# Performance work log

Hardware: AMD Instinct MI355X
Metric: run time of the kernel (lower is better)

## Reference

```python
import jax, jax.numpy as jnp
import numpy as np

A0 = 0.5291772105638411
KE = 14.399645351950548
KEHALF = KE / 2.0

def softplus_inverse(x):
    x = np.asarray(x, dtype=np.float64)
    return np.float32(x + np.log(-np.expm1(-x)))

def setup_inputs() -> dict:
    key = jax.random.key(0)
    k1, k2, k3, k4 = jax.random.split(key, 4)
    B, N, K = 16, 8192, 128
    neighbors = jax.random.randint(k1, (B, N, K), 0, N, dtype=jnp.int64)
    neighbor_mask = jnp.ones((B, N, K), dtype=jnp.float32)
    # atomic numbers in [1, 94] (Z=0 would break d/dp of Z**p)
    atomic_numbers = jax.random.randint(k2, (B, N), 0, 94, dtype=jnp.int64) + 1
    # distances scaled into a physical range [0.5, 5.5) Angstrom to avoid r->0
    distances = jax.random.uniform(k3, (B, N, K), dtype=jnp.float32) * 5.0 + 0.5
    p = lambda v: jnp.full((1,), softplus_inverse(v), dtype=jnp.float32)
    return {
        'neighbors': neighbors,
        'neighbor_mask': neighbor_mask,
        'atomic_numbers': atomic_numbers,
        'distances': distances,
        'adiv': p(1.0 / (0.8854 * A0)),
        'apow': p(0.23),
        'c1': p(0.1818), 'c2': p(0.5099), 'c3': p(0.2802), 'c4': p(0.02817),
        'a1': p(3.2), 'a2': p(0.9423), 'a3': p(0.4028), 'a4': p(0.2016),
    }

def reference(neighbors, neighbor_mask, atomic_numbers, distances,
              adiv, apow, c1, c2, c3, c4, a1, a2, a3, a4):
    sp = jax.nn.softplus
    Zf = atomic_numbers.astype(jnp.float32)            # [B, N]
    zpow = Zf ** sp(apow)                              # [B, N]
    # per-batch gather over neighbor index (sparse edge list, no NxN build)
    gather = jax.vmap(lambda v, nb: v[nb])             # ([N],[N,K]) -> [N,K]
    zpow_j = gather(zpow, neighbors)                   # [B, N, K]
    a = (zpow[:, :, None] + zpow_j) * sp(adiv) * neighbor_mask
    zizj = Zf[:, :, None] * gather(Zf, neighbors) * neighbor_mask
    c1s, c2s, c3s, c4s = sp(c1), sp(c2), sp(c3), sp(c4)
    csum = c1s + c2s + c3s + c4s
    f = (c1s / csum) * jnp.exp(-sp(a1) * a * distances) \
      + (c2s / csum) * jnp.exp(-sp(a2) * a * distances) \
      + (c3s / csum) * jnp.exp(-sp(a3) * a * distances) \
      + (c4s / csum) * jnp.exp(-sp(a4) * a * distances)
    corr = jnp.where(neighbor_mask != 0,
                     KEHALF * f * zizj / distances,
                     jnp.zeros_like(distances))        # [B, N, K]
    return jnp.sum(corr, axis=(-1, -2))[:, None]       # [B, 1]
```

## Files before the change

### kernel.cpp

```cpp
#include <hip/hip_runtime.h>


#define KEHALF_F 7.199822675975274f
#define LOG2E_F  1.4426950408889634f
#define EPI      256
#define WAVES_PB 2
#define BUFB     3072

__device__ __forceinline__ float softplus_f(float x) {
    return (x > 20.f) ? x : log1pf(__expf(x));
}

__global__ void zbl_pre(const int* __restrict__ zn,
                        const float* __restrict__ adiv,
                        const float* __restrict__ apow,
                        const float* __restrict__ c1, const float* __restrict__ c2,
                        const float* __restrict__ c3, const float* __restrict__ c4,
                        const float* __restrict__ a1, const float* __restrict__ a2,
                        const float* __restrict__ a3, const float* __restrict__ a4,
                        unsigned short* __restrict__ packed, float* __restrict__ scal,
                        int total_atoms)
{
    int i = blockIdx.x * blockDim.x + threadIdx.x;
    const float spa = softplus_f(apow[0]);
    const float sad = softplus_f(adiv[0]);
    const float qb  = sad;
    const float qmax = sad * __expf(spa * __logf(94.f));
    const float qs  = (qmax - qb) * (1.f / 511.f);
    if (i == 0) {
        float s1 = softplus_f(c1[0]), s2 = softplus_f(c2[0]);
        float s3 = softplus_f(c3[0]), s4 = softplus_f(c4[0]);
        float inv = KEHALF_F / (s1 + s2 + s3 + s4);
        scal[0] = sad;
        scal[1] = s1 * inv;
        scal[2] = s2 * inv;
        scal[3] = s3 * inv;
        scal[4] = s4 * inv;
        scal[5] = -softplus_f(a1[0]) * LOG2E_F;
        scal[6] = -softplus_f(a2[0]) * LOG2E_F;
        scal[7] = -softplus_f(a3[0]) * LOG2E_F;
        scal[8] = -softplus_f(a4[0]) * LOG2E_F;
        scal[9]  = qb;
        scal[10] = qs;
    }
    if (i < total_atoms) {
        unsigned int Z = (unsigned int)zn[i];
        float Zf = (float)Z;
        float zps = sad * __expf(spa * __logf(Zf));
        float qf = (zps - qb) / qs;
        int q = (int)(qf + 0.5f);
        if (q < 0) q = 0;
        if (q > 511) q = 511;
        packed[i] = (unsigned short)(((unsigned)q << 7) | (Z & 0x7Fu));
    }
}

extern __shared__ unsigned short tab[];

#define STAGE(bufp, it) do {                                                      \
    const int*   _n = nb + (size_t)(it) * EPI + lane * 4;                         \
    const float* _m = mk + (size_t)(it) * EPI + lane * 4;                         \
    const float* _d = ds + (size_t)(it) * EPI + lane * 4;                         \
    __builtin_amdgcn_global_load_lds(                                             \
        (const __attribute__((address_space(1))) void*)_n,                        \
        (__attribute__((address_space(3))) void*)(bufp), 16, 0, 0);               \
    __builtin_amdgcn_global_load_lds(                                             \
        (const __attribute__((address_space(1))) void*)_m,                        \
        (__attribute__((address_space(3))) void*)((bufp) + 1024), 16, 0, 0);      \
    __builtin_amdgcn_global_load_lds(                                             \
        (const __attribute__((address_space(1))) void*)_d,                        \
        (__attribute__((address_space(3))) void*)((bufp) + 2048), 16, 0, 0);      \
} while (0)

__global__ __launch_bounds__(128) void zbl_main_a(
        const int*            __restrict__ neighbors,
        const float*          __restrict__ mask,
        const float*          __restrict__ dist,
        const unsigned short* __restrict__ packed,
        const float*          __restrict__ scal,
        float*                __restrict__ out,
        int N, int kshift, int epb, int iters)
{
    __shared__ char  stage[WAVES_PB][2][BUFB];
    __shared__ float wsum[WAVES_PB];

    const int tid  = threadIdx.x;
    const int w    = tid >> 6;
    const int lane = tid & 63;
    const int b    = blockIdx.y;

    const float w1 = scal[1], w2 = scal[2], w3 = scal[3], w4 = scal[4];
    const float e1 = scal[5], e2 = scal[6], e3 = scal[7], e4 = scal[8];
    const float qb = scal[9], qs = scal[10];

    const size_t batch_base = (size_t)b * epb;
    const int    wave_span  = iters * EPI;
    const int    r_wave     = (blockIdx.x * WAVES_PB + w) * wave_span;
    const int*   nb = neighbors + batch_base + r_wave;
    const float* mk = mask      + batch_base + r_wave;
    const float* ds = dist      + batch_base + r_wave;

    char* buf0 = &stage[w][0][0];
    char* buf1 = &stage[w][1][0];

    STAGE(buf0, 0);
    if (iters > 1) STAGE(buf1, 1);

    {
        const uint4* s4 = (const uint4*)(packed + (size_t)b * N);
        uint4* t4 = (uint4*)tab;
        const int n8 = N >> 3;
        for (int i = tid; i < n8; i += 128) t4[i] = s4[i];
    }
    __syncthreads();

    float acc = 0.f;
    for (int it = 0; it < iters; ++it) {
        char* bp = (it & 1) ? buf1 : buf0;
        if (it == iters - 1) { asm volatile("s_waitcnt vmcnt(0)" ::: "memory"); }
        else                 { asm volatile("s_waitcnt vmcnt(3)" ::: "memory"); }

        const int4   i4 = *(const int4*)  (bp + lane * 16);
        const float4 m4 = *(const float4*)(bp + 1024 + lane * 16);
        const float4 d4 = *(const float4*)(bp + 2048 + lane * 16);
        asm volatile("s_waitcnt lgkmcnt(0)" ::: "memory");
        if (it + 2 < iters) STAGE(bp, it + 2);

        const int r = r_wave + it * EPI + lane * 4;
        const unsigned int wi = tab[r >> kshift];
        const float zpi = fmaf((float)(wi >> 7), qs, qb);
        const float Zi  = (float)(wi & 0x7Fu);

        const int   idxs[4] = { i4.x, i4.y, i4.z, i4.w };
        const float mm[4]   = { m4.x, m4.y, m4.z, m4.w };
        const float dd[4]   = { d4.x, d4.y, d4.z, d4.w };

        #pragma unroll
        for (int u = 0; u < 4; ++u) {
            const unsigned int wj = tab[idxs[u]];
            const float zpj = fmaf((float)(wj >> 7), qs, qb);
            const float Zj  = (float)(wj & 0x7Fu);
            const float m = mm[u], d = dd[u];
            const float a  = (zpi + zpj) * m;
            const float zz = Zi * Zj * m;
            const float ad = a * d;
            const float f = w1 * exp2f(e1 * ad)
                          + w2 * exp2f(e2 * ad)
                          + w3 * exp2f(e3 * ad)
                          + w4 * exp2f(e4 * ad);
            const float g = f * zz * __builtin_amdgcn_rcpf(d);
            acc += (m != 0.f) ? g : 0.f;
        }
    }

    #pragma unroll
    for (int off = 32; off > 0; off >>= 1) acc += __shfl_down(acc, off);
    if (lane == 0) wsum[w] = acc;
    __syncthreads();
    if (tid == 0) atomicAdd(&out[b], wsum[0] + wsum[1]);
}

__global__ void zbl_fallback(const int* __restrict__ neighbors,
                             const float* __restrict__ mask,
                             const float* __restrict__ dist,
                             const unsigned short* __restrict__ packed,
                             const float* __restrict__ scal,
                             float* __restrict__ out,
                             int N, int K, int epb, int total_edges)
{
    const int e = blockIdx.x * blockDim.x + threadIdx.x;
    if (e >= total_edges) return;
    const float w1 = scal[1], w2 = scal[2], w3 = scal[3], w4 = scal[4];
    const float e1 = scal[5], e2 = scal[6], e3 = scal[7], e4 = scal[8];
    const float qb = scal[9], qs = scal[10];
    const int b = e / epb;
    const int n = (e - b * epb) / K;
    const unsigned int wi = packed[(size_t)b * N + n];
    const unsigned int wj = packed[(size_t)b * N + neighbors[e]];
    const float zpi = fmaf((float)(wi >> 7), qs, qb);
    const float zpj = fmaf((float)(wj >> 7), qs, qb);
    const float Zi = (float)(wi & 0x7Fu), Zj = (float)(wj & 0x7Fu);
    const float m = mask[e], d = dist[e];
    const float a  = (zpi + zpj) * m;
    const float ad = a * d;
    const float f = w1 * exp2f(e1 * ad) + w2 * exp2f(e2 * ad)
                  + w3 * exp2f(e3 * ad) + w4 * exp2f(e4 * ad);
    const float corr = (m != 0.f) ? (f * Zi * Zj * m / d) : 0.f;
    if (corr != 0.f) atomicAdd(&out[b], corr);
}

extern "C" void kernel_launch(void* const* d_in, const int* in_sizes, int n_in,
                              void* d_out, int out_size, void* d_ws, size_t ws_size,
                              hipStream_t stream) {
    const int*   neighbors = (const int*)  d_in[0];
    const float* nb_mask   = (const float*)d_in[1];
    const int*   zn        = (const int*)  d_in[2];
    const float* dist      = (const float*)d_in[3];
    const float* adiv = (const float*)d_in[4];
    const float* apow = (const float*)d_in[5];
    const float* c1 = (const float*)d_in[6];
    const float* c2 = (const float*)d_in[7];
    const float* c3 = (const float*)d_in[8];
    const float* c4 = (const float*)d_in[9];
    const float* a1 = (const float*)d_in[10];
    const float* a2 = (const float*)d_in[11];
    const float* a3 = (const float*)d_in[12];
    const float* a4 = (const float*)d_in[13];

    const int total_edges = in_sizes[0];
    const int total_atoms = in_sizes[2];
    const int B = out_size;
    const int N = total_atoms / B;
    const int K = total_edges / total_atoms;
    const int epb = N * K;

    float*          scal   = (float*)d_ws;
    unsigned short* packed = (unsigned short*)((char*)d_ws + 64);

    hipMemsetAsync(d_out, 0, (size_t)out_size * sizeof(float), stream);

    {
        const int threads = 256;
        const int blocks = (total_atoms + threads - 1) / threads;
        zbl_pre<<<blocks, threads, 0, stream>>>(zn, adiv, apow, c1, c2, c3, c4,
                                                a1, a2, a3, a4,
                                                packed, scal, total_atoms);
    }

    int kshift = 0;
    while ((1 << kshift) < K && kshift < 30) kshift++;
    const bool kpow2 = ((1 << kshift) == K);

    const int bpb = 64;
    const bool fast = kpow2 && (K % 4 == 0) &&
                      (epb % (bpb * WAVES_PB * EPI) == 0) &&
                      (N % 8 == 0) &&
                      ((size_t)N * 2 <= 40960) &&
                      ((size_t)(64 + (size_t)total_atoms * 2) <= ws_size);
    if (fast) {
        const int iters = epb / (bpb * WAVES_PB * EPI);
        dim3 grid(bpb, B);
        zbl_main_a<<<grid, 128, N * sizeof(unsigned short), stream>>>(
            neighbors, nb_mask, dist, packed, scal, (float*)d_out,
            N, kshift, epb, iters);
    } else {
        const int threads = 256;
        const int blocks = (total_edges + threads - 1) / threads;
        zbl_fallback<<<blocks, threads, 0, stream>>>(
            neighbors, nb_mask, dist, packed, scal, (float*)d_out,
            N, K, epb, total_edges);
    }
}
```

Before: 61.06 us.

## Replace four-exponential screening sum with LDS lookup table and linear interpolation

A new pre-kernel tabulates the weighted four-exponential screening function, with KEHALF folded in, over a fixed range of a*d. It stores the value and forward difference at 1024 points. The main kernel copies this table into shared memory and replaces four exp2 calls per edge with one LDS read and one FMA. It also drops the global_load_lds double-buffer pipeline in favour of 256-thread blocks that prefetch the next pass into registers. This cuts transcendental ALU work per edge, but adds interpolation error, a clamp at a*d=80, and more LDS traffic and bank conflicts from random table reads.

```diff
diff --git a/kernel.cpp b/kernel.cpp
--- a/kernel.cpp
+++ b/kernel.cpp
@@ -3,9 +3,10 @@
 
 #define KEHALF_F 7.199822675975274f
 #define LOG2E_F  1.4426950408889634f
-#define EPI      256
-#define WAVES_PB 2
-#define BUFB     3072
+#define LUTN     1024
+#define LUT_ADMAX 80.0f
+#define EPP      1024
+#define PASSES   8
 
 __device__ __forceinline__ float softplus_f(float x) {
     return (x > 20.f) ? x : log1pf(__expf(x));
@@ -55,109 +56,115 @@
     }
 }
 
-extern __shared__ unsigned short tab[];
-
-#define STAGE(bufp, it) do {                                                      \
-    const int*   _n = nb + (size_t)(it) * EPI + lane * 4;                         \
-    const float* _m = mk + (size_t)(it) * EPI + lane * 4;                         \
-    const float* _d = ds + (size_t)(it) * EPI + lane * 4;                         \
-    __builtin_amdgcn_global_load_lds(                                             \
-        (const __attribute__((address_space(1))) void*)_n,                        \
-        (__attribute__((address_space(3))) void*)(bufp), 16, 0, 0);               \
-    __builtin_amdgcn_global_load_lds(                                             \
-        (const __attribute__((address_space(1))) void*)_m,                        \
-        (__attribute__((address_space(3))) void*)((bufp) + 1024), 16, 0, 0);      \
-    __builtin_amdgcn_global_load_lds(                                             \
-        (const __attribute__((address_space(1))) void*)_d,                        \
-        (__attribute__((address_space(3))) void*)((bufp) + 2048), 16, 0, 0);      \
-} while (0)
-
-__global__ __launch_bounds__(128) void zbl_main_a(
+__global__ void zbl_lut_k(const float* __restrict__ c1, const float* __restrict__ c2,
+                          const float* __restrict__ c3, const float* __restrict__ c4,
+                          const float* __restrict__ a1, const float* __restrict__ a2,
+                          const float* __restrict__ a3, const float* __restrict__ a4,
+                          float2* __restrict__ lut)
+{
+    int i = blockIdx.x * blockDim.x + threadIdx.x;
+    if (i >= LUTN) return;
+    float s1 = softplus_f(c1[0]), s2 = softplus_f(c2[0]);
+    float s3 = softplus_f(c3[0]), s4 = softplus_f(c4[0]);
+    float inv = KEHALF_F / (s1 + s2 + s3 + s4);
+    float w1 = s1 * inv, w2 = s2 * inv, w3 = s3 * inv, w4 = s4 * inv;
+    float g1 = -softplus_f(a1[0]), g2 = -softplus_f(a2[0]);
+    float g3 = -softplus_f(a3[0]), g4 = -softplus_f(a4[0]);
+    const float h = LUT_ADMAX / (float)(LUTN - 1);
+    float x0 = (float)i * h, x1 = x0 + h;
+    float f0 = w1 * __expf(g1 * x0) + w2 * __expf(g2 * x0)
+             + w3 * __expf(g3 * x0) + w4 * __expf(g4 * x0);
+    float f1 = w1 * __expf(g1 * x1) + w2 * __expf(g2 * x1)
+             + w3 * __expf(g3 * x1) + w4 * __expf(g4 * x1);
+    lut[i] = make_float2(f0, f1 - f0);
+}
+
+extern __shared__ char smem[];
+
+__global__ __launch_bounds__(256, 6) void zbl_main_l(
         const int*            __restrict__ neighbors,
         const float*          __restrict__ mask,
         const float*          __restrict__ dist,
         const unsigned short* __restrict__ packed,
+        const float2*         __restrict__ lutg,
         const float*          __restrict__ scal,
         float*                __restrict__ out,
-        int N, int kshift, int epb, int iters)
-{
-    __shared__ char  stage[WAVES_PB][2][BUFB];
-    __shared__ float wsum[WAVES_PB];
-
-    const int tid  = threadIdx.x;
-    const int w    = tid >> 6;
-    const int lane = tid & 63;
-    const int b    = blockIdx.y;
-
-    const float w1 = scal[1], w2 = scal[2], w3 = scal[3], w4 = scal[4];
-    const float e1 = scal[5], e2 = scal[6], e3 = scal[7], e4 = scal[8];
-    const float qb = scal[9], qs = scal[10];
-
-    const size_t batch_base = (size_t)b * epb;
-    const int    wave_span  = iters * EPI;
-    const int    r_wave     = (blockIdx.x * WAVES_PB + w) * wave_span;
-    const int*   nb = neighbors + batch_base + r_wave;
-    const float* mk = mask      + batch_base + r_wave;
-    const float* ds = dist      + batch_base + r_wave;
-
-    char* buf0 = &stage[w][0][0];
-    char* buf1 = &stage[w][1][0];
-
-    STAGE(buf0, 0);
-    if (iters > 1) STAGE(buf1, 1);
+        int N, int kshift, int epb, int passes)
+{
+    unsigned short* tab = (unsigned short*)smem;
+    float2*         lut = (float2*)(smem + (size_t)N * 2);
+
+    const int tid = threadIdx.x;
+    const int b   = blockIdx.y;
+    const int span = passes << 10;
+    const int r0   = blockIdx.x * span + tid * 4;
+    const size_t base = (size_t)b * epb + r0;
+    const int*   nb = neighbors + base;
+    const float* mk = mask      + base;
+    const float* ds = dist      + base;
+
+    int4   ci = *(const int4*)nb;
+    float4 cm = *(const float4*)mk;
+    float4 cd = *(const float4*)ds;
 
     {
         const uint4* s4 = (const uint4*)(packed + (size_t)b * N);
         uint4* t4 = (uint4*)tab;
-        const int n8 = N >> 3;
-        for (int i = tid; i < n8; i += 128) t4[i] = s4[i];
-    }
+        for (int i = tid, e = N >> 3; i < e; i += 256) t4[i] = s4[i];
+        const uint4* l4 = (const uint4*)lutg;
+        uint4* d4 = (uint4*)lut;
+        for (int i = tid, e = LUTN >> 1; i < e; i += 256) d4[i] = l4[i];
+    }
+    const float qb = scal[9], qs = scal[10];
     __syncthreads();
 
+    const float lscale = (float)(LUTN - 1) * (1.0f / LUT_ADMAX);
+    const float tmax   = (float)(LUTN - 1) - 1.0f;
+
     float acc = 0.f;
-    for (int it = 0; it < iters; ++it) {
-        char* bp = (it & 1) ? buf1 : buf0;
-        if (it == iters - 1) { asm volatile("s_waitcnt vmcnt(0)" ::: "memory"); }
-        else                 { asm volatile("s_waitcnt vmcnt(3)" ::: "memory"); }
-
-        const int4   i4 = *(const int4*)  (bp + lane * 16);
-        const float4 m4 = *(const float4*)(bp + 1024 + lane * 16);
-        const float4 d4 = *(const float4*)(bp + 2048 + lane * 16);
-        asm volatile("s_waitcnt lgkmcnt(0)" ::: "memory");
-        if (it + 2 < iters) STAGE(bp, it + 2);
-
-        const int r = r_wave + it * EPI + lane * 4;
-        const unsigned int wi = tab[r >> kshift];
+
+    auto compute = [&](int g, int4 gi, float4 gm, float4 gd) {
+        const unsigned int wi = tab[(r0 + (g << 10)) >> kshift];
         const float zpi = fmaf((float)(wi >> 7), qs, qb);
         const float Zi  = (float)(wi & 0x7Fu);
-
-        const int   idxs[4] = { i4.x, i4.y, i4.z, i4.w };
-        const float mm[4]   = { m4.x, m4.y, m4.z, m4.w };
-        const float dd[4]   = { d4.x, d4.y, d4.z, d4.w };
-
+        const int   idxs[4] = { gi.x, gi.y, gi.z, gi.w };
+        const float mm[4]   = { gm.x, gm.y, gm.z, gm.w };
+        const float dd[4]   = { gd.x, gd.y, gd.z, gd.w };
         #pragma unroll
         for (int u = 0; u < 4; ++u) {
             const unsigned int wj = tab[idxs[u]];
             const float zpj = fmaf((float)(wj >> 7), qs, qb);
             const float Zj  = (float)(wj & 0x7Fu);
             const float m = mm[u], d = dd[u];
-            const float a  = (zpi + zpj) * m;
             const float zz = Zi * Zj * m;
-            const float ad = a * d;
-            const float f = w1 * exp2f(e1 * ad)
-                          + w2 * exp2f(e2 * ad)
-                          + w3 * exp2f(e3 * ad)
-                          + w4 * exp2f(e4 * ad);
-            const float g = f * zz * __builtin_amdgcn_rcpf(d);
-            acc += (m != 0.f) ? g : 0.f;
+            const float ad = (zpi + zpj) * (m * d);
+            float t = fminf(ad * lscale, tmax);
+            const int   it = (int)t;
+            const float fr = t - (float)it;
+            const float2 lv = lut[it];
+            const float f  = fmaf(fr, lv.y, lv.x);
+            const float gc = f * zz * __builtin_amdgcn_rcpf(d);
+            acc += (m != 0.f) ? gc : 0.f;
         }
-    }
+    };
+
+    for (int g = 0; g < passes - 1; ++g) {
+        const int go = (g + 1) << 10;
+        int4   ni = *(const int4*)(nb + go);
+        float4 nm = *(const float4*)(mk + go);
+        float4 nd = *(const float4*)(ds + go);
+        compute(g, ci, cm, cd);
+        ci = ni; cm = nm; cd = nd;
+    }
+    compute(passes - 1, ci, cm, cd);
 
     #pragma unroll
     for (int off = 32; off > 0; off >>= 1) acc += __shfl_down(acc, off);
+    __shared__ float wsum[4];
+    const int w = tid >> 6, lane = tid & 63;
     if (lane == 0) wsum[w] = acc;
     __syncthreads();
-    if (tid == 0) atomicAdd(&out[b], wsum[0] + wsum[1]);
+    if (tid == 0) atomicAdd(&out[b], wsum[0] + wsum[1] + wsum[2] + wsum[3]);
 }
 
 __global__ void zbl_fallback(const int* __restrict__ neighbors,
@@ -216,6 +223,8 @@
 
     float*          scal   = (float*)d_ws;
     unsigned short* packed = (unsigned short*)((char*)d_ws + 64);
+    const size_t lut_off   = 64 + (size_t)total_atoms * 2;
+    float2*         lutg   = (float2*)((char*)d_ws + ((lut_off + 15) & ~(size_t)15));
 
     hipMemsetAsync(d_out, 0, (size_t)out_size * sizeof(float), stream);
 
@@ -226,23 +235,23 @@
                                                 a1, a2, a3, a4,
                                                 packed, scal, total_atoms);
     }
+    zbl_lut_k<<<LUTN / 256, 256, 0, stream>>>(c1, c2, c3, c4, a1, a2, a3, a4, lutg);
 
     int kshift = 0;
     while ((1 << kshift) < K && kshift < 30) kshift++;
     const bool kpow2 = ((1 << kshift) == K);
 
-    const int bpb = 64;
-    const bool fast = kpow2 && (K % 4 == 0) &&
-                      (epb % (bpb * WAVES_PB * EPI) == 0) &&
-                      (N % 8 == 0) &&
-                      ((size_t)N * 2 <= 40960) &&
-                      ((size_t)(64 + (size_t)total_atoms * 2) <= ws_size);
+    const size_t lds_bytes = (size_t)N * 2 + (size_t)LUTN * 8;
+    const bool fast = kpow2 && (K % 4 == 0) && (N % 8 == 0) &&
+                      (epb % (EPP * PASSES) == 0) &&
+                      (lds_bytes <= 64 * 1024) &&
+                      (((lut_off + 15) & ~(size_t)15) + LUTN * 8 <= ws_size);
     if (fast) {
-        const int iters = epb / (bpb * WAVES_PB * EPI);
+        const int bpb = epb / (EPP * PASSES);
         dim3 grid(bpb, B);
-        zbl_main_a<<<grid, 128, N * sizeof(unsigned short), stream>>>(
-            neighbors, nb_mask, dist, packed, scal, (float*)d_out,
-            N, kshift, epb, iters);
+        zbl_main_l<<<grid, 256, lds_bytes, stream>>>(
+            neighbors, nb_mask, dist, packed, lutg, scal, (float*)d_out,
+            N, kshift, epb, PASSES);
     } else {
         const int threads = 256;
         const int blocks = (total_edges + threads - 1) / threads;
```

Measured after the change: 67.80 us. +11.0%, slower.

## Restructure main kernel into 8-wave blocks with 4-deep LDS staging pipeline

Applied to the files above, without the earlier changes.

Replaces the 2-wave, double-buffered, 16-byte-per-lane staging with 512-thread blocks of 8 waves, each running a 4-deep ring of 4-byte-per-lane async global-to-LDS loads processing 64 edges per iteration. The atomic-number table copy is issued before the staging loads so it overlaps them, and the grid is resized so each wave handles 32 iterations. The aim is more memory-level parallelism and better latency hiding through deeper prefetch and more waves per block, at the cost of narrower per-lane loads and more loop iterations with extra waitcnt overhead. The cross-wave reduction now reuses staging LDS after an extra barrier.

```diff
diff --git a/kernel.cpp b/kernel.cpp
--- a/kernel.cpp
+++ b/kernel.cpp
@@ -3,9 +3,10 @@
 
 #define KEHALF_F 7.199822675975274f
 #define LOG2E_F  1.4426950408889634f
-#define EPI      256
-#define WAVES_PB 2
-#define BUFB     3072
+#define DEPTH    4
+#define GRAN     64
+#define WPB      8
+#define SLOTB    768
 
 __device__ __forceinline__ float softplus_f(float x) {
     return (x > 20.f) ? x : log1pf(__expf(x));
@@ -57,22 +58,39 @@
 
 extern __shared__ unsigned short tab[];
 
-#define STAGE(bufp, it) do {                                                      \
-    const int*   _n = nb + (size_t)(it) * EPI + lane * 4;                         \
-    const float* _m = mk + (size_t)(it) * EPI + lane * 4;                         \
-    const float* _d = ds + (size_t)(it) * EPI + lane * 4;                         \
+#define STAGE(slotp, it) do {                                                     \
+    const int off = (it) * GRAN + lane;                                           \
     __builtin_amdgcn_global_load_lds(                                             \
-        (const __attribute__((address_space(1))) void*)_n,                        \
-        (__attribute__((address_space(3))) void*)(bufp), 16, 0, 0);               \
+        (const __attribute__((address_space(1))) void*)(nb_ + off),               \
+        (__attribute__((address_space(3))) void*)(slotp), 4, 0, 0);               \
     __builtin_amdgcn_global_load_lds(                                             \
-        (const __attribute__((address_space(1))) void*)_m,                        \
-        (__attribute__((address_space(3))) void*)((bufp) + 1024), 16, 0, 0);      \
+        (const __attribute__((address_space(1))) void*)(mk_ + off),               \
+        (__attribute__((address_space(3))) void*)((slotp) + 256), 4, 0, 0);       \
     __builtin_amdgcn_global_load_lds(                                             \
-        (const __attribute__((address_space(1))) void*)_d,                        \
-        (__attribute__((address_space(3))) void*)((bufp) + 2048), 16, 0, 0);      \
+        (const __attribute__((address_space(1))) void*)(ds_ + off),               \
+        (__attribute__((address_space(3))) void*)((slotp) + 512), 4, 0, 0);       \
 } while (0)
 
-__global__ __launch_bounds__(128) void zbl_main_a(
+#define CONSUME(sp, it) do {                                                      \
+    const int   ji = *(const int*)  ((sp) + (lane << 2));                         \
+    const float mm = *(const float*)((sp) + 256 + (lane << 2));                   \
+    const float dd = *(const float*)((sp) + 512 + (lane << 2));                   \
+    const int r = rw + ((it) << 6) + lane;                                        \
+    const unsigned int wi_ = tab[r >> kshift];                                    \
+    const unsigned int wj_ = tab[ji];                                             \
+    const float zpi = fmaf((float)(wi_ >> 7), qs, qb);                            \
+    const float Zi  = (float)(wi_ & 0x7Fu);                                       \
+    const float zpj = fmaf((float)(wj_ >> 7), qs, qb);                            \
+    const float Zj  = (float)(wj_ & 0x7Fu);                                       \
+    const float zz = Zi * Zj * mm;                                                \
+    const float ad = (zpi + zpj) * (mm * dd);                                     \
+    const float f = w1 * exp2f(e1 * ad) + w2 * exp2f(e2 * ad)                     \
+                  + w3 * exp2f(e3 * ad) + w4 * exp2f(e4 * ad);                    \
+    const float gc = f * zz * __builtin_amdgcn_rcpf(dd);                          \
+    acc += (mm != 0.f) ? gc : 0.f;                                                \
+} while (0)
+
+__global__ __launch_bounds__(512, 8) void zbl_main7(
         const int*            __restrict__ neighbors,
         const float*          __restrict__ mask,
         const float*          __restrict__ dist,
@@ -81,83 +99,107 @@
         float*                __restrict__ out,
         int N, int kshift, int epb, int iters)
 {
-    __shared__ char  stage[WAVES_PB][2][BUFB];
-    __shared__ float wsum[WAVES_PB];
+    __shared__ char stage[WPB][DEPTH][SLOTB];
 
     const int tid  = threadIdx.x;
     const int w    = tid >> 6;
     const int lane = tid & 63;
     const int b    = blockIdx.y;
 
+    const int rw = (blockIdx.x * WPB + w) * (iters * GRAN);
+    const size_t ebase = (size_t)b * epb + (size_t)rw;
+    const int*   nb_ = neighbors + ebase;
+    const float* mk_ = mask      + ebase;
+    const float* ds_ = dist      + ebase;
+
+    const uint4* s4 = (const uint4*)(packed + (size_t)b * N);
+    const int n8 = N >> 3;
+    uint4 tv0, tv1;
+    const bool h0 = (tid < n8);
+    const bool h1 = (tid + 512 < n8);
+    if (h0) tv0 = s4[tid];
+    if (h1) tv1 = s4[tid + 512];
+
+    {
+        char* sp0 = &stage[w][0][0];
+        STAGE(sp0, 0);
+        char* sp1 = &stage[w][1][0];
+        STAGE(sp1, 1);
+        char* sp2 = &stage[w][2][0];
+        STAGE(sp2, 2);
+        char* sp3 = &stage[w][3][0];
+        STAGE(sp3, 3);
+    }
+
+    {
+        uint4* t4 = (uint4*)tab;
+        if (h0) t4[tid] = tv0;
+        if (h1) t4[tid + 512] = tv1;
+    }
     const float w1 = scal[1], w2 = scal[2], w3 = scal[3], w4 = scal[4];
     const float e1 = scal[5], e2 = scal[6], e3 = scal[7], e4 = scal[8];
     const float qb = scal[9], qs = scal[10];
-
-    const size_t batch_base = (size_t)b * epb;
-    const int    wave_span  = iters * EPI;
-    const int    r_wave     = (blockIdx.x * WAVES_PB + w) * wave_span;
-    const int*   nb = neighbors + batch_base + r_wave;
-    const float* mk = mask      + batch_base + r_wave;
-    const float* ds = dist      + batch_base + r_wave;
-
-    char* buf0 = &stage[w][0][0];
-    char* buf1 = &stage[w][1][0];
-
-    STAGE(buf0, 0);
-    if (iters > 1) STAGE(buf1, 1);
-
-    {
-        const uint4* s4 = (const uint4*)(packed + (size_t)b * N);
-        uint4* t4 = (uint4*)tab;
-        const int n8 = N >> 3;
-        for (int i = tid; i < n8; i += 128) t4[i] = s4[i];
-    }
     __syncthreads();
 
     float acc = 0.f;
-    for (int it = 0; it < iters; ++it) {
-        char* bp = (it & 1) ? buf1 : buf0;
-        if (it == iters - 1) { asm volatile("s_waitcnt vmcnt(0)" ::: "memory"); }
-        else                 { asm volatile("s_waitcnt vmcnt(3)" ::: "memory"); }
-
-        const int4   i4 = *(const int4*)  (bp + lane * 16);
-        const float4 m4 = *(const float4*)(bp + 1024 + lane * 16);
-        const float4 d4 = *(const float4*)(bp + 2048 + lane * 16);
+    int it = 0;
+
+    for (; it < iters - DEPTH; ++it) {
+        asm volatile("s_waitcnt vmcnt(9)" ::: "memory");
+        char* sp = &stage[w][it & (DEPTH - 1)][0];
+        const int   ji = *(const int*)  (sp + (lane << 2));
+        const float mm = *(const float*)(sp + 256 + (lane << 2));
+        const float dd = *(const float*)(sp + 512 + (lane << 2));
         asm volatile("s_waitcnt lgkmcnt(0)" ::: "memory");
-        if (it + 2 < iters) STAGE(bp, it + 2);
-
-        const int r = r_wave + it * EPI + lane * 4;
-        const unsigned int wi = tab[r >> kshift];
-        const float zpi = fmaf((float)(wi >> 7), qs, qb);
-        const float Zi  = (float)(wi & 0x7Fu);
-
-        const int   idxs[4] = { i4.x, i4.y, i4.z, i4.w };
-        const float mm[4]   = { m4.x, m4.y, m4.z, m4.w };
-        const float dd[4]   = { d4.x, d4.y, d4.z, d4.w };
-
-        #pragma unroll
-        for (int u = 0; u < 4; ++u) {
-            const unsigned int wj = tab[idxs[u]];
-            const float zpj = fmaf((float)(wj >> 7), qs, qb);
-            const float Zj  = (float)(wj & 0x7Fu);
-            const float m = mm[u], d = dd[u];
-            const float a  = (zpi + zpj) * m;
-            const float zz = Zi * Zj * m;
-            const float ad = a * d;
-            const float f = w1 * exp2f(e1 * ad)
-                          + w2 * exp2f(e2 * ad)
-                          + w3 * exp2f(e3 * ad)
-                          + w4 * exp2f(e4 * ad);
-            const float g = f * zz * __builtin_amdgcn_rcpf(d);
-            acc += (m != 0.f) ? g : 0.f;
-        }
+        STAGE(sp, it + DEPTH);
+        const int r = rw + (it << 6) + lane;
+        const unsigned int wi_ = tab[r >> kshift];
+        const unsigned int wj_ = tab[ji];
+        const float zpi = fmaf((float)(wi_ >> 7), qs, qb);
+        const float Zi  = (float)(wi_ & 0x7Fu);
+        const float zpj = fmaf((float)(wj_ >> 7), qs, qb);
+        const float Zj  = (float)(wj_ & 0x7Fu);
+        const float zz = Zi * Zj * mm;
+        const float ad = (zpi + zpj) * (mm * dd);
+        const float f = w1 * exp2f(e1 * ad) + w2 * exp2f(e2 * ad)
+                      + w3 * exp2f(e3 * ad) + w4 * exp2f(e4 * ad);
+        const float gc = f * zz * __builtin_amdgcn_rcpf(dd);
+        acc += (mm != 0.f) ? gc : 0.f;
+    }
+
+    {
+        asm volatile("s_waitcnt vmcnt(9)" ::: "memory");
+        char* sp = &stage[w][it & (DEPTH - 1)][0];
+        CONSUME(sp, it); ++it;
+    }
+    {
+        asm volatile("s_waitcnt vmcnt(6)" ::: "memory");
+        char* sp = &stage[w][it & (DEPTH - 1)][0];
+        CONSUME(sp, it); ++it;
+    }
+    {
+        asm volatile("s_waitcnt vmcnt(3)" ::: "memory");
+        char* sp = &stage[w][it & (DEPTH - 1)][0];
+        CONSUME(sp, it); ++it;
+    }
+    {
+        asm volatile("s_waitcnt vmcnt(0)" ::: "memory");
+        char* sp = &stage[w][it & (DEPTH - 1)][0];
+        CONSUME(sp, it); ++it;
     }
 
     #pragma unroll
     for (int off = 32; off > 0; off >>= 1) acc += __shfl_down(acc, off);
-    if (lane == 0) wsum[w] = acc;
     __syncthreads();
-    if (tid == 0) atomicAdd(&out[b], wsum[0] + wsum[1]);
+    float* wred = (float*)&stage[0][0][0];
+    if (lane == 0) wred[w] = acc;
+    __syncthreads();
+    if (tid == 0) {
+        float t = 0.f;
+        #pragma unroll
+        for (int i = 0; i < WPB; ++i) t += wred[i];
+        atomicAdd(&out[b], t);
+    }
 }
 
 __global__ void zbl_fallback(const int* __restrict__ neighbors,
@@ -231,18 +273,18 @@
     while ((1 << kshift) < K && kshift < 30) kshift++;
     const bool kpow2 = ((1 << kshift) == K);
 
-    const int bpb = 64;
-    const bool fast = kpow2 && (K % 4 == 0) &&
-                      (epb % (bpb * WAVES_PB * EPI) == 0) &&
-                      (N % 8 == 0) &&
-                      ((size_t)N * 2 <= 40960) &&
+    const int ITERS = 32;
+    const int span_block = WPB * GRAN * ITERS;
+    const size_t lds_dyn = (size_t)N * 2;
+    const bool fast = kpow2 && (N % 8 == 0) && (N <= 8192) &&
+                      (epb % span_block == 0) &&
                       ((size_t)(64 + (size_t)total_atoms * 2) <= ws_size);
     if (fast) {
-        const int iters = epb / (bpb * WAVES_PB * EPI);
+        const int bpb = epb / span_block;
         dim3 grid(bpb, B);
-        zbl_main_a<<<grid, 128, N * sizeof(unsigned short), stream>>>(
+        zbl_main7<<<grid, 512, lds_dyn, stream>>>(
             neighbors, nb_mask, dist, packed, scal, (float*)d_out,
-            N, kshift, epb, iters);
+            N, kshift, epb, ITERS);
     } else {
         const int threads = 256;
         const int blocks = (total_edges + threads - 1) / threads;
```

Result: faster. 53.91 us (-11.7%).
